# Optimization experiments

Measured on AMD Instinct MI355X. Metric: run time of the kernel, lower is better.

Reference implementation:

```python
import jax, jax.numpy as jnp
import numpy as np

NUM_HEADS = 16

def setup_inputs() -> dict:
    key = jax.random.key(0)
    k1, k2, k3 = jax.random.split(key, 3)
    B, N, E = 4, 2048, 1024
    x = jax.random.normal(k1, (B, N, E), dtype=jnp.float32)
    W_qkv = jax.random.normal(k2, (3 * E, E), dtype=jnp.float32) * (E ** -0.5)
    W_proj = jax.random.normal(k3, (E, E), dtype=jnp.float32) * (E ** -0.5)
    return {"x": x, "W_qkv": W_qkv, "W_proj": W_proj}

def reference(x, W_qkv, W_proj):
    B, N, E = x.shape
    H = NUM_HEADS
    hd = E // H
    scale = hd ** 0.5
    # qkv linear (no bias): [B,N,3E]; the original's transpose/reshape dance is
    # equivalent to a contiguous split into Q,K,V of size E each.
    qkv = jnp.einsum('bne,fe->bnf', x, W_qkv)
    q, k, v = jnp.split(qkv, 3, axis=-1)
    # [B,N,E] -> [B,H,N,hd]
    def to_heads(t):
        return t.reshape(B, N, H, hd).transpose(0, 2, 1, 3)
    q = to_heads(q) / scale
    k = to_heads(k)
    v = to_heads(v)
    attn = jax.nn.softmax(jnp.einsum('bhnd,bhmd->bhnm', q, k), axis=-1)
    sv = jnp.einsum('bhnm,bhmd->bhnd', attn, v)  # [B,H,N,hd]
    sv = sv.transpose(0, 2, 1, 3).reshape(B, N, E)
    out = jnp.einsum('bne,fe->bnf', sv, W_proj)
    return (out, sv)
```

## Files before the change

kernel.cpp:

```cpp
#include <hip/hip_runtime.h>
#include <stdint.h>

typedef unsigned short u16;
typedef __attribute__((ext_vector_type(8))) short bf16x8;
typedef __attribute__((ext_vector_type(4))) float f32x4;

__device__ __forceinline__ u16 f2bf(float f) {
    union { float f; uint32_t u; } v; v.f = f;
    return (u16)((v.u + 0x7FFFu + ((v.u >> 16) & 1u)) >> 16);
}

__device__ __forceinline__ float fexp2(float x) {
    return __builtin_amdgcn_exp2f(x);
}

__device__ __forceinline__ void gload16(const void* g, void* l) {
    __builtin_amdgcn_global_load_lds(
        (__attribute__((address_space(1))) void*)(g),
        (__attribute__((address_space(3))) void*)(l),
        16, 0, 0);
}

__global__ __launch_bounds__(256) void cast_kernel(
        const float* __restrict__ x, const float* __restrict__ wqkv,
        const float* __restrict__ wproj,
        u16* __restrict__ xb, u16* __restrict__ wqb, u16* __restrict__ wpb) {
    const int NX4 = 2097152;
    const int NW4 = 786432;
    int i = blockIdx.x * 256 + threadIdx.x;
    const float* src; u16* dst; int j;
    if (i < NX4) { src = x; dst = xb; j = i; }
    else if (i < NX4 + NW4) { src = wqkv; dst = wqb; j = i - NX4; }
    else { src = wproj; dst = wpb; j = i - NX4 - NW4; }
    float4 v = ((const float4*)src)[j];
    ushort4 o;
    o.x = f2bf(v.x); o.y = f2bf(v.y); o.z = f2bf(v.z); o.w = f2bf(v.w);
    ((ushort4*)dst)[j] = o;
}

template<int MODE>
__global__ __launch_bounds__(256) void gemm_nt(
        const u16* __restrict__ A, const u16* __restrict__ Bm, int K,
        u16* __restrict__ oq, u16* __restrict__ ok, u16* __restrict__ ov,
        float* __restrict__ oc) {
    __shared__ __align__(16) u16 As[128 * 64];
    __shared__ __align__(16) u16 Bs[128 * 64];
    const int t = threadIdx.x;
    const int lane = t & 63, w = t >> 6;
    const int wr = w >> 1, wc = w & 1;
    const int q4 = lane >> 4, c = lane & 15;
    const int rowBase = blockIdx.y * 128;
    const int colBase = blockIdx.x * 128;
    const int lrow = lane >> 3;
    const int lcol = (lane & 7) * 8;

    f32x4 z = {0.f, 0.f, 0.f, 0.f};
    f32x4 acc[4][4];
#pragma unroll
    for (int i = 0; i < 4; i++)
#pragma unroll
        for (int j = 0; j < 4; j++) acc[i][j] = z;

    for (int k0 = 0; k0 < K; k0 += 64) {
        __syncthreads();
#pragma unroll
        for (int s = 0; s < 4; s++) {
            int ch = w * 4 + s;
            int row = ch * 8 + lrow;
            gload16(A + (size_t)(rowBase + row) * K + k0 + lcol, &As[ch * 512]);
            gload16(Bm + (size_t)(colBase + row) * K + k0 + lcol, &Bs[ch * 512]);
        }
        __syncthreads();
#pragma unroll
        for (int kk = 0; kk < 2; kk++) {
            bf16x8 af[4], bfr[4];
#pragma unroll
            for (int mt = 0; mt < 4; mt++)
                af[mt] = *(const bf16x8*)&As[(wr * 64 + mt * 16 + c) * 64 + kk * 32 + q4 * 8];
#pragma unroll
            for (int nt = 0; nt < 4; nt++)
                bfr[nt] = *(const bf16x8*)&Bs[(wc * 64 + nt * 16 + c) * 64 + kk * 32 + q4 * 8];
#pragma unroll
            for (int mt = 0; mt < 4; mt++)
#pragma unroll
                for (int nt = 0; nt < 4; nt++)
                    acc[mt][nt] = __builtin_amdgcn_mfma_f32_16x16x32_bf16(
                        af[mt], bfr[nt], acc[mt][nt], 0, 0, 0);
        }
    }

    const float QSCALE = 0.125f * 1.44269504088896341f;
#pragma unroll
    for (int mt = 0; mt < 4; mt++) {
#pragma unroll
        for (int nt = 0; nt < 4; nt++) {
#pragma unroll
            for (int r = 0; r < 4; r++) {
                int gRow = rowBase + wr * 64 + mt * 16 + q4 * 4 + r;
                int gCol = colBase + wc * 64 + nt * 16 + c;
                float v = acc[mt][nt][r];
                if (MODE == 0) {
                    int b = gRow >> 11, n = gRow & 2047;
                    int region = gCol >> 10, e = gCol & 1023;
                    int h = e >> 6, d = e & 63;
                    if (region == 0)
                        oq[(size_t)(((b << 4) + h) * 2048 + n) * 64 + d] = f2bf(v * QSCALE);
                    else if (region == 1)
                        ok[(size_t)(((b << 4) + h) * 2048 + n) * 64 + d] = f2bf(v);
                    else
                        ov[(size_t)(((b << 4) + h) * 64 + d) * 2048 + n] = f2bf(v);
                } else {
                    oc[(size_t)gRow * 1024 + gCol] = v;
                }
            }
        }
    }
}

__global__ __launch_bounds__(256) void attn_kernel(
        const u16* __restrict__ Q, const u16* __restrict__ Kg,
        const u16* __restrict__ Vt, float* __restrict__ svf, u16* __restrict__ svb) {
    __shared__ __align__(16) u16 Ks[64 * 72];
    __shared__ __align__(16) u16 Vs[64 * 72];
    __shared__ __align__(16) u16 Ps[4][32 * 72];
    const int t = threadIdx.x;
    const int lane = t & 63, w = t >> 6;
    const int q4 = lane >> 4, c = lane & 15;
    const int bh = blockIdx.y;
    const int qBase = blockIdx.x * 128 + w * 32;
    const u16* Qh = Q + (size_t)bh * 2048 * 64;
    const u16* Kp = Kg + (size_t)bh * 2048 * 64;
    const u16* Vp = Vt + (size_t)bh * 64 * 2048;

    bf16x8 aq[2][2];
#pragma unroll
    for (int mt = 0; mt < 2; mt++) {
        aq[mt][0] = *(const bf16x8*)(Qh + (size_t)(qBase + mt * 16 + c) * 64 + q4 * 8);
        aq[mt][1] = *(const bf16x8*)(Qh + (size_t)(qBase + mt * 16 + c) * 64 + 32 + q4 * 8);
    }

    f32x4 z = {0.f, 0.f, 0.f, 0.f};
    f32x4 O[2][4];
    float lsum[2][4];
#pragma unroll
    for (int mt = 0; mt < 2; mt++)
#pragma unroll
        for (int i = 0; i < 4; i++) { O[mt][i] = z; lsum[mt][i] = 0.f; }

    for (int kv0 = 0; kv0 < 2048; kv0 += 64) {
        bf16x8 rk[2], rv[2];
#pragma unroll
        for (int i = 0; i < 2; i++) {
            int ch = t + 256 * i;
            int row = ch >> 3, cc = ch & 7;
            rk[i] = *(const bf16x8*)(Kp + (size_t)(kv0 + row) * 64 + cc * 8);
            rv[i] = *(const bf16x8*)(Vp + (size_t)row * 2048 + kv0 + cc * 8);
        }
        __syncthreads();
#pragma unroll
        for (int i = 0; i < 2; i++) {
            int ch = t + 256 * i;
            int row = ch >> 3, cc = ch & 7;
            *(bf16x8*)(Ks + row * 72 + cc * 8) = rk[i];
            *(bf16x8*)(Vs + row * 72 + cc * 8) = rv[i];
        }
        __syncthreads();

        f32x4 S[2][4];
#pragma unroll
        for (int ct = 0; ct < 4; ct++) {
            bf16x8 k0 = *(const bf16x8*)(Ks + (ct * 16 + c) * 72 + q4 * 8);
            bf16x8 k1 = *(const bf16x8*)(Ks + (ct * 16 + c) * 72 + 32 + q4 * 8);
#pragma unroll
            for (int mt = 0; mt < 2; mt++) {
                f32x4 s = __builtin_amdgcn_mfma_f32_16x16x32_bf16(aq[mt][0], k0, z, 0, 0, 0);
                s = __builtin_amdgcn_mfma_f32_16x16x32_bf16(aq[mt][1], k1, s, 0, 0, 0);
                S[mt][ct] = s;
            }
        }
#pragma unroll
        for (int mt = 0; mt < 2; mt++)
#pragma unroll
            for (int ct = 0; ct < 4; ct++)
#pragma unroll
                for (int r = 0; r < 4; r++) {
                    float e = fexp2(S[mt][ct][r]);
                    lsum[mt][r] += e;
                    Ps[w][(mt * 16 + q4 * 4 + r) * 72 + ct * 16 + c] = f2bf(e);
                }
        bf16x8 pa[2][2];
#pragma unroll
        for (int mt = 0; mt < 2; mt++) {
            pa[mt][0] = *(const bf16x8*)&Ps[w][(mt * 16 + c) * 72 + q4 * 8];
            pa[mt][1] = *(const bf16x8*)&Ps[w][(mt * 16 + c) * 72 + 32 + q4 * 8];
        }
#pragma unroll
        for (int ct = 0; ct < 4; ct++) {
            bf16x8 v0 = *(const bf16x8*)(Vs + (ct * 16 + c) * 72 + q4 * 8);
            bf16x8 v1 = *(const bf16x8*)(Vs + (ct * 16 + c) * 72 + 32 + q4 * 8);
#pragma unroll
            for (int mt = 0; mt < 2; mt++) {
                O[mt][ct] = __builtin_amdgcn_mfma_f32_16x16x32_bf16(pa[mt][0], v0, O[mt][ct], 0, 0, 0);
                O[mt][ct] = __builtin_amdgcn_mfma_f32_16x16x32_bf16(pa[mt][1], v1, O[mt][ct], 0, 0, 0);
            }
        }
    }

#pragma unroll
    for (int mt = 0; mt < 2; mt++)
#pragma unroll
        for (int r = 0; r < 4; r++) {
            float s = lsum[mt][r];
#pragma unroll
            for (int off = 1; off < 16; off <<= 1)
                s += __shfl_xor(s, off);
            lsum[mt][r] = 1.0f / s;
        }

    int b = bh >> 4, h = bh & 15;
#pragma unroll
    for (int mt = 0; mt < 2; mt++) {
#pragma unroll
        for (int ct = 0; ct < 4; ct++) {
#pragma unroll
            for (int r = 0; r < 4; r++) {
                int n = qBase + mt * 16 + q4 * 4 + r;
                int e = h * 64 + ct * 16 + c;
                float v = O[mt][ct][r] * lsum[mt][r];
                size_t idx = (size_t)(b * 2048 + n) * 1024 + e;
                svf[idx] = v;
                svb[idx] = f2bf(v);
            }
        }
    }
}

extern "C" void kernel_launch(void* const* d_in, const int* in_sizes, int n_in,
                              void* d_out, int out_size, void* d_ws, size_t ws_size,
                              hipStream_t stream) {
    const float* x = (const float*)d_in[0];
    const float* wqkv = (const float*)d_in[1];
    const float* wproj = (const float*)d_in[2];
    float* out = (float*)d_out;
    float* svf = out + 8388608;

    u16* xb  = (u16*)d_ws;
    u16* wqb = xb + 8388608;
    u16* wpb = wqb + 3145728;
    u16* qb  = wpb + 1048576;
    u16* kb  = qb + 8388608;
    u16* vtb = kb + 8388608;
    u16* svb = xb;

    cast_kernel<<<dim3(12288), dim3(256), 0, stream>>>(x, wqkv, wproj, xb, wqb, wpb);
    gemm_nt<0><<<dim3(24, 64), dim3(256), 0, stream>>>(xb, wqb, 1024, qb, kb, vtb, nullptr);
    attn_kernel<<<dim3(16, 64), dim3(256), 0, stream>>>(qb, kb, vtb, svf, svb);
    gemm_nt<1><<<dim3(8, 64), dim3(256), 0, stream>>>(svb, wpb, 1024, nullptr, nullptr, nullptr, out);
}
```

Measured before the change: 341.6 us.

## Swizzle LDS tiles, transpose attention MFMA to keep P in registers, double-buffer KV

GEMM LDS tiles now use an XOR swizzle to avoid bank conflicts. The V-output epilogue transposes through LDS so it can write 16-byte vector stores. The attention kernel computes S transposed (K as the A operand), so the exp'd probabilities feed the PV MFMA (16x16x16) straight from registers and no longer go through a per-wave LDS buffer. It also double-buffers K/V tiles with async global-to-LDS loads and writes the output as vectorised float4 and bf16x4 stores. Several independent changes land together, and the extra transposes and swizzling add indexing complexity.

```diff
diff --git a/kernel.cpp b/kernel.cpp
--- a/kernel.cpp
+++ b/kernel.cpp
@@ -3,12 +3,19 @@
 
 typedef unsigned short u16;
 typedef __attribute__((ext_vector_type(8))) short bf16x8;
+typedef __attribute__((ext_vector_type(4))) short bf16x4;
 typedef __attribute__((ext_vector_type(4))) float f32x4;
 
 __device__ __forceinline__ u16 f2bf(float f) {
     union { float f; uint32_t u; } v; v.f = f;
     return (u16)((v.u + 0x7FFFu + ((v.u >> 16) & 1u)) >> 16);
 }
+
+__device__ __forceinline__ uint32_t pack2bf(float a, float b) {
+    return (uint32_t)f2bf(a) | ((uint32_t)f2bf(b) << 16);
+}
+
+#define MFMA16(a, b, c) __builtin_amdgcn_mfma_f32_16x16x16bf16_1k(a, b, c, 0, 0, 0)
 
 __device__ __forceinline__ float fexp2(float x) {
     return __builtin_amdgcn_exp2f(x);
@@ -43,16 +50,18 @@
         const u16* __restrict__ A, const u16* __restrict__ Bm, int K,
         u16* __restrict__ oq, u16* __restrict__ ok, u16* __restrict__ ov,
         float* __restrict__ oc) {
-    __shared__ __align__(16) u16 As[128 * 64];
-    __shared__ __align__(16) u16 Bs[128 * 64];
+    __shared__ __align__(16) u16 smem[17408];
+    u16* As = smem;
+    u16* Bs = smem + 8192;
     const int t = threadIdx.x;
     const int lane = t & 63, w = t >> 6;
     const int wr = w >> 1, wc = w & 1;
     const int q4 = lane >> 4, c = lane & 15;
+    const int lrow = lane >> 3;
+    const int lc = lane & 7;
     const int rowBase = blockIdx.y * 128;
     const int colBase = blockIdx.x * 128;
-    const int lrow = lane >> 3;
-    const int lcol = (lane & 7) * 8;
+    const int c7 = c & 7;
 
     f32x4 z = {0.f, 0.f, 0.f, 0.f};
     f32x4 acc[4][4];
@@ -67,8 +76,9 @@
         for (int s = 0; s < 4; s++) {
             int ch = w * 4 + s;
             int row = ch * 8 + lrow;
-            gload16(A + (size_t)(rowBase + row) * K + k0 + lcol, &As[ch * 512]);
-            gload16(Bm + (size_t)(colBase + row) * K + k0 + lcol, &Bs[ch * 512]);
+            int cg = (lc ^ lrow) * 8;
+            gload16(A + (size_t)(rowBase + row) * K + k0 + cg, &As[ch * 512]);
+            gload16(Bm + (size_t)(colBase + row) * K + k0 + cg, &Bs[ch * 512]);
         }
         __syncthreads();
 #pragma unroll
@@ -76,10 +86,10 @@
             bf16x8 af[4], bfr[4];
 #pragma unroll
             for (int mt = 0; mt < 4; mt++)
-                af[mt] = *(const bf16x8*)&As[(wr * 64 + mt * 16 + c) * 64 + kk * 32 + q4 * 8];
+                af[mt] = *(const bf16x8*)&As[(wr * 64 + mt * 16 + c) * 64 + ((kk * 4 + q4) ^ c7) * 8];
 #pragma unroll
             for (int nt = 0; nt < 4; nt++)
-                bfr[nt] = *(const bf16x8*)&Bs[(wc * 64 + nt * 16 + c) * 64 + kk * 32 + q4 * 8];
+                bfr[nt] = *(const bf16x8*)&Bs[(wc * 64 + nt * 16 + c) * 64 + ((kk * 4 + q4) ^ c7) * 8];
 #pragma unroll
             for (int mt = 0; mt < 4; mt++)
 #pragma unroll
@@ -90,29 +100,62 @@
     }
 
     const float QSCALE = 0.125f * 1.44269504088896341f;
-#pragma unroll
-    for (int mt = 0; mt < 4; mt++) {
-#pragma unroll
-        for (int nt = 0; nt < 4; nt++) {
-#pragma unroll
-            for (int r = 0; r < 4; r++) {
-                int gRow = rowBase + wr * 64 + mt * 16 + q4 * 4 + r;
+
+    if (MODE == 1) {
+#pragma unroll
+        for (int mt = 0; mt < 4; mt++)
+#pragma unroll
+            for (int nt = 0; nt < 4; nt++)
+#pragma unroll
+                for (int r = 0; r < 4; r++)
+                    oc[(size_t)(rowBase + wr * 64 + mt * 16 + q4 * 4 + r) * 1024 +
+                       colBase + wc * 64 + nt * 16 + c] = acc[mt][nt][r];
+        return;
+    }
+
+    int region = colBase >> 10;
+    if (region < 2) {
+        float s0 = (region == 0) ? QSCALE : 1.0f;
+        u16* outp = (region == 0) ? oq : ok;
+#pragma unroll
+        for (int mt = 0; mt < 4; mt++) {
+#pragma unroll
+            for (int nt = 0; nt < 4; nt++) {
+                int gRow = rowBase + wr * 64 + mt * 16 + q4 * 4;
                 int gCol = colBase + wc * 64 + nt * 16 + c;
-                float v = acc[mt][nt][r];
-                if (MODE == 0) {
-                    int b = gRow >> 11, n = gRow & 2047;
-                    int region = gCol >> 10, e = gCol & 1023;
-                    int h = e >> 6, d = e & 63;
-                    if (region == 0)
-                        oq[(size_t)(((b << 4) + h) * 2048 + n) * 64 + d] = f2bf(v * QSCALE);
-                    else if (region == 1)
-                        ok[(size_t)(((b << 4) + h) * 2048 + n) * 64 + d] = f2bf(v);
-                    else
-                        ov[(size_t)(((b << 4) + h) * 64 + d) * 2048 + n] = f2bf(v);
-                } else {
-                    oc[(size_t)gRow * 1024 + gCol] = v;
-                }
-            }
+                int bb = gRow >> 11, n = gRow & 2047;
+                int e = gCol & 1023, h = e >> 6, d = e & 63;
+                u16* dst = outp + ((size_t)(((bb << 4) + h) * 2048 + n)) * 64 + d;
+                uint32_t p0 = pack2bf(acc[mt][nt][0] * s0, acc[mt][nt][1] * s0);
+                uint32_t p1 = pack2bf(acc[mt][nt][2] * s0, acc[mt][nt][3] * s0);
+                dst[0]   = (u16)p0;  dst[64]  = (u16)(p0 >> 16);
+                dst[128] = (u16)p1;  dst[192] = (u16)(p1 >> 16);
+            }
+        }
+    } else {
+        __syncthreads();
+        u16* LT = smem;
+#pragma unroll
+        for (int mt = 0; mt < 4; mt++) {
+#pragma unroll
+            for (int nt = 0; nt < 4; nt++) {
+                int col = wc * 64 + nt * 16 + c;
+                int row = wr * 64 + mt * 16 + q4 * 4;
+                uint2 pp;
+                pp.x = pack2bf(acc[mt][nt][0], acc[mt][nt][1]);
+                pp.y = pack2bf(acc[mt][nt][2], acc[mt][nt][3]);
+                *(uint2*)&LT[col * 136 + row] = pp;
+            }
+        }
+        __syncthreads();
+        int bb = rowBase >> 11, n0 = rowBase & 2047;
+#pragma unroll
+        for (int i = 0; i < 8; i++) {
+            int col = (t >> 4) + 16 * i;
+            int rc = t & 15;
+            bf16x8 val = *(const bf16x8*)&LT[col * 136 + rc * 8];
+            int e = (colBase + col) & 1023, h = e >> 6, d = e & 63;
+            *(bf16x8*)&ov[((size_t)((bb << 4) + h) * 64 + d) * 2048 + n0 + rc * 8] = val;
         }
     }
 }
@@ -120,117 +163,108 @@
 __global__ __launch_bounds__(256) void attn_kernel(
         const u16* __restrict__ Q, const u16* __restrict__ Kg,
         const u16* __restrict__ Vt, float* __restrict__ svf, u16* __restrict__ svb) {
-    __shared__ __align__(16) u16 Ks[64 * 72];
-    __shared__ __align__(16) u16 Vs[64 * 72];
-    __shared__ __align__(16) u16 Ps[4][32 * 72];
+    __shared__ __align__(16) u16 smem[2][2][4096];
     const int t = threadIdx.x;
     const int lane = t & 63, w = t >> 6;
     const int q4 = lane >> 4, c = lane & 15;
+    const int lrow = lane >> 3, lc = lane & 7;
+    const int c7 = c & 7;
     const int bh = blockIdx.y;
     const int qBase = blockIdx.x * 128 + w * 32;
     const u16* Qh = Q + (size_t)bh * 2048 * 64;
     const u16* Kp = Kg + (size_t)bh * 2048 * 64;
     const u16* Vp = Vt + (size_t)bh * 64 * 2048;
 
-    bf16x8 aq[2][2];
+    bf16x8 bq[2][2];
 #pragma unroll
     for (int mt = 0; mt < 2; mt++) {
-        aq[mt][0] = *(const bf16x8*)(Qh + (size_t)(qBase + mt * 16 + c) * 64 + q4 * 8);
-        aq[mt][1] = *(const bf16x8*)(Qh + (size_t)(qBase + mt * 16 + c) * 64 + 32 + q4 * 8);
+        bq[mt][0] = *(const bf16x8*)(Qh + (size_t)(qBase + mt * 16 + c) * 64 + q4 * 8);
+        bq[mt][1] = *(const bf16x8*)(Qh + (size_t)(qBase + mt * 16 + c) * 64 + 32 + q4 * 8);
     }
 
     f32x4 z = {0.f, 0.f, 0.f, 0.f};
     f32x4 O[2][4];
-    float lsum[2][4];
+    float lsum[2] = {0.f, 0.f};
 #pragma unroll
     for (int mt = 0; mt < 2; mt++)
 #pragma unroll
-        for (int i = 0; i < 4; i++) { O[mt][i] = z; lsum[mt][i] = 0.f; }
-
-    for (int kv0 = 0; kv0 < 2048; kv0 += 64) {
-        bf16x8 rk[2], rv[2];
-#pragma unroll
-        for (int i = 0; i < 2; i++) {
-            int ch = t + 256 * i;
-            int row = ch >> 3, cc = ch & 7;
-            rk[i] = *(const bf16x8*)(Kp + (size_t)(kv0 + row) * 64 + cc * 8);
-            rv[i] = *(const bf16x8*)(Vp + (size_t)row * 2048 + kv0 + cc * 8);
-        }
-        __syncthreads();
-#pragma unroll
-        for (int i = 0; i < 2; i++) {
-            int ch = t + 256 * i;
-            int row = ch >> 3, cc = ch & 7;
-            *(bf16x8*)(Ks + row * 72 + cc * 8) = rk[i];
-            *(bf16x8*)(Vs + row * 72 + cc * 8) = rv[i];
-        }
-        __syncthreads();
-
-        f32x4 S[2][4];
-#pragma unroll
-        for (int ct = 0; ct < 4; ct++) {
-            bf16x8 k0 = *(const bf16x8*)(Ks + (ct * 16 + c) * 72 + q4 * 8);
-            bf16x8 k1 = *(const bf16x8*)(Ks + (ct * 16 + c) * 72 + 32 + q4 * 8);
+        for (int dt = 0; dt < 4; dt++) O[mt][dt] = z;
+
+#pragma unroll
+    for (int s = 0; s < 2; s++) {
+        int r2 = w * 16 + s * 8 + lrow;
+        int cg = (lc ^ lrow) * 8;
+        gload16(Kp + (size_t)r2 * 64 + cg, &smem[0][0][(w * 16 + s * 8) * 64]);
+        gload16(Vp + (size_t)r2 * 2048 + cg, &smem[0][1][(w * 16 + s * 8) * 64]);
+    }
+    __syncthreads();
+
+    for (int i = 0; i < 32; i++) {
+        int buf = i & 1;
+        if (i < 31) {
+            int kvn = (i + 1) * 64;
+#pragma unroll
+            for (int s = 0; s < 2; s++) {
+                int r2 = w * 16 + s * 8 + lrow;
+                int cg = (lc ^ lrow) * 8;
+                gload16(Kp + (size_t)(kvn + r2) * 64 + cg, &smem[buf ^ 1][0][(w * 16 + s * 8) * 64]);
+                gload16(Vp + (size_t)r2 * 2048 + kvn + cg, &smem[buf ^ 1][1][(w * 16 + s * 8) * 64]);
+            }
+        }
+        const u16* Ksb = smem[buf][0];
+        const u16* Vsb = smem[buf][1];
+#pragma unroll
+        for (int kvt = 0; kvt < 4; kvt++) {
+            bf16x8 ka0 = *(const bf16x8*)&Ksb[(kvt * 16 + c) * 64 + ((q4) ^ c7) * 8];
+            bf16x8 ka1 = *(const bf16x8*)&Ksb[(kvt * 16 + c) * 64 + ((4 + q4) ^ c7) * 8];
+            bf16x4 Pf[2];
 #pragma unroll
             for (int mt = 0; mt < 2; mt++) {
-                f32x4 s = __builtin_amdgcn_mfma_f32_16x16x32_bf16(aq[mt][0], k0, z, 0, 0, 0);
-                s = __builtin_amdgcn_mfma_f32_16x16x32_bf16(aq[mt][1], k1, s, 0, 0, 0);
-                S[mt][ct] = s;
-            }
-        }
-#pragma unroll
-        for (int mt = 0; mt < 2; mt++)
-#pragma unroll
-            for (int ct = 0; ct < 4; ct++)
-#pragma unroll
-                for (int r = 0; r < 4; r++) {
-                    float e = fexp2(S[mt][ct][r]);
-                    lsum[mt][r] += e;
-                    Ps[w][(mt * 16 + q4 * 4 + r) * 72 + ct * 16 + c] = f2bf(e);
-                }
-        bf16x8 pa[2][2];
-#pragma unroll
-        for (int mt = 0; mt < 2; mt++) {
-            pa[mt][0] = *(const bf16x8*)&Ps[w][(mt * 16 + c) * 72 + q4 * 8];
-            pa[mt][1] = *(const bf16x8*)&Ps[w][(mt * 16 + c) * 72 + 32 + q4 * 8];
-        }
-#pragma unroll
-        for (int ct = 0; ct < 4; ct++) {
-            bf16x8 v0 = *(const bf16x8*)(Vs + (ct * 16 + c) * 72 + q4 * 8);
-            bf16x8 v1 = *(const bf16x8*)(Vs + (ct * 16 + c) * 72 + 32 + q4 * 8);
-#pragma unroll
-            for (int mt = 0; mt < 2; mt++) {
-                O[mt][ct] = __builtin_amdgcn_mfma_f32_16x16x32_bf16(pa[mt][0], v0, O[mt][ct], 0, 0, 0);
-                O[mt][ct] = __builtin_amdgcn_mfma_f32_16x16x32_bf16(pa[mt][1], v1, O[mt][ct], 0, 0, 0);
-            }
-        }
-    }
-
-#pragma unroll
-    for (int mt = 0; mt < 2; mt++)
-#pragma unroll
-        for (int r = 0; r < 4; r++) {
-            float s = lsum[mt][r];
-#pragma unroll
-            for (int off = 1; off < 16; off <<= 1)
-                s += __shfl_xor(s, off);
-            lsum[mt][r] = 1.0f / s;
-        }
+                f32x4 s = __builtin_amdgcn_mfma_f32_16x16x32_bf16(ka0, bq[mt][0], z, 0, 0, 0);
+                s = __builtin_amdgcn_mfma_f32_16x16x32_bf16(ka1, bq[mt][1], s, 0, 0, 0);
+                float e0 = fexp2(s[0]), e1 = fexp2(s[1]), e2 = fexp2(s[2]), e3 = fexp2(s[3]);
+                lsum[mt] += (e0 + e1) + (e2 + e3);
+                union { uint2 u; bf16x4 v; } uu;
+                uu.u.x = pack2bf(e0, e1);
+                uu.u.y = pack2bf(e2, e3);
+                Pf[mt] = uu.v;
+            }
+#pragma unroll
+            for (int dt = 0; dt < 4; dt++) {
+                int chunk = (kvt * 2 + (q4 >> 1)) ^ c7;
+                bf16x4 va = *(const bf16x4*)&Vsb[(dt * 16 + c) * 64 + chunk * 8 + (q4 & 1) * 4];
+#pragma unroll
+                for (int mt = 0; mt < 2; mt++)
+                    O[mt][dt] = MFMA16(va, Pf[mt], O[mt][dt]);
+            }
+        }
+        __syncthreads();
+    }
+
+#pragma unroll
+    for (int mt = 0; mt < 2; mt++) {
+        float s = lsum[mt];
+        s += __shfl_xor(s, 16);
+        s += __shfl_xor(s, 32);
+        lsum[mt] = 1.0f / s;
+    }
 
     int b = bh >> 4, h = bh & 15;
 #pragma unroll
     for (int mt = 0; mt < 2; mt++) {
-#pragma unroll
-        for (int ct = 0; ct < 4; ct++) {
-#pragma unroll
-            for (int r = 0; r < 4; r++) {
-                int n = qBase + mt * 16 + q4 * 4 + r;
-                int e = h * 64 + ct * 16 + c;
-                float v = O[mt][ct][r] * lsum[mt][r];
-                size_t idx = (size_t)(b * 2048 + n) * 1024 + e;
-                svf[idx] = v;
-                svb[idx] = f2bf(v);
-            }
+        int n = qBase + mt * 16 + c;
+        float rl = lsum[mt];
+#pragma unroll
+        for (int dt = 0; dt < 4; dt++) {
+            float4 o4;
+            o4.x = O[mt][dt][0] * rl; o4.y = O[mt][dt][1] * rl;
+            o4.z = O[mt][dt][2] * rl; o4.w = O[mt][dt][3] * rl;
+            size_t base = (size_t)(b * 2048 + n) * 1024 + h * 64 + dt * 16 + q4 * 4;
+            *(float4*)&svf[base] = o4;
+            uint2 pb;
+            pb.x = pack2bf(o4.x, o4.y);
+            pb.y = pack2bf(o4.z, o4.w);
+            *(uint2*)&svb[base] = pb;
         }
     }
 }
```

Result: faster. 287.3 us (-15.9%).
